# Performance work log

Measured on AMD Instinct MI355X. Metric: run time of the kernel, lower is better.

The kernel has to match this reference:

```python
import jax, jax.numpy as jnp
import numpy as np

LOSS_WEIGHT = 1.0  # init kwarg


def _cdist2(a, b):
    # Euclidean (p=2) pairwise distances via Gram trick: avoids [n,m,d] tensor.
    d2 = (jnp.sum(a * a, axis=1)[:, None]
          + jnp.sum(b * b, axis=1)[None, :]
          - 2.0 * (a @ b.T))
    return jnp.sqrt(jnp.maximum(d2, 0.0))


def _clamp_comb(f, g):
    # Composition of clamp maps x -> clip(x, lo, hi); g is applied after f.
    lf, hf = f
    lg, hg = g
    return jnp.clip(lf, lg, hg), jnp.clip(hf, lg, hg)


def _frechet(pred, target):
    c = _cdist2(pred, target)                      # [n, m]
    # First DP row: running max of c[0, :].
    row0 = jax.lax.associative_scan(jnp.maximum, c[0])

    def row_update(prev, c_row):
        # ca[i,j] = max(min(ca[i-1,j], ca[i,j-1], ca[i-1,j-1]), c[i,j])
        # For fixed i this is d[j] = clip(d[j-1], lo=c[i,j], hi=max(b[j], c[i,j]))
        # with b[j] = min(prev[j], prev[j-1]); clamp composition is associative,
        # so the whole row is a parallel associative scan (wavefront-free form).
        d0 = jnp.maximum(prev[0], c_row[0])        # ca[i,0]
        lo = c_row[1:]
        hi = jnp.maximum(jnp.minimum(prev[1:], prev[:-1]), lo)
        lo_all = jnp.concatenate([d0[None], lo])   # element 0 is the constant map d0
        hi_all = jnp.concatenate([d0[None], hi])
        lo_s, _ = jax.lax.associative_scan(_clamp_comb, (lo_all, hi_all))
        return lo_s, None

    last_row, _ = jax.lax.scan(row_update, row0, c[1:])
    return last_row[-1]


def setup_inputs() -> dict:
    key = jax.random.key(0)
    k1, k2 = jax.random.split(key)
    pred = jax.random.uniform(k1, (4096, 128), dtype=jnp.float32)
    target = jax.random.uniform(k2, (4096, 128), dtype=jnp.float32)
    return {"pred": pred, "target": target}


def reference(pred, target):
    return LOSS_WEIGHT * _frechet(pred, target)
```

## Files before the change

### kernel.cpp

```cpp
#include <hip/hip_runtime.h>

typedef unsigned short u16;
typedef unsigned int u32;
typedef __bf16 bf16x8 __attribute__((ext_vector_type(8)));
typedef float f32x4 __attribute__((ext_vector_type(4)));

#define N 4096
#define KD 128
#define NSTRIP 16
#define G 4
#define W 256
#define ROWB 512
#define CH 64
#define NCHUNK 64
#define NBLK 65
#define WINROWS 192
#define LDSROWS 200
#define TOTSTEP 4159
#define HUGEV 3.0e38f
#define TS 128
#define PADK 136
#define PSTRIDE 32

__device__ __forceinline__ u16 f2bf(float v) {
  u32 u = __float_as_uint(v);
  u += 0x7fffu + ((u >> 16) & 1u);
  return (u16)(u >> 16);
}
__device__ __forceinline__ float bf2f(u16 b) { return __uint_as_float(((u32)b) << 16); }
__device__ __forceinline__ float bfround(float v) { return bf2f(f2bf(v)); }

__device__ __forceinline__ float dpp_shr1(float oldv, float src) {
  return __int_as_float(__builtin_amdgcn_update_dpp(
      __float_as_int(oldv), __float_as_int(src), 0x138, 0xF, 0xF, false));
}

__device__ __forceinline__ void gload_lds16(const void* g, void* l) {
  __builtin_amdgcn_global_load_lds((const __attribute__((address_space(1))) u32*)g,
                                   (__attribute__((address_space(3))) u32*)l, 16, 0, 0);
}

__global__ __launch_bounds__(256) void norms_kernel(const float* __restrict__ pred,
                                                    const float* __restrict__ tgt,
                                                    float* __restrict__ na, float* __restrict__ nb,
                                                    int* __restrict__ prog) {
  if (blockIdx.x == 0 && threadIdx.x < NSTRIP) prog[threadIdx.x * PSTRIDE] = 0;
  int gw = blockIdx.x * 4 + (threadIdx.x >> 6);
  int lane = threadIdx.x & 63;
  const float* base = (gw < N) ? (pred + (size_t)gw * KD) : (tgt + (size_t)(gw - N) * KD);
  float2 v = ((const float2*)base)[lane];
  float x = bfround(v.x), y = bfround(v.y);
  float s = x * x + y * y;
  #pragma unroll
  for (int off = 32; off > 0; off >>= 1) s += __shfl_xor(s, off);
  if (lane == 0) { if (gw < N) na[gw] = s; else nb[gw - N] = s; }
}

__global__ __launch_bounds__(256) void gemm_kernel(const float* __restrict__ A, const float* __restrict__ B,
                                                   const float* __restrict__ na, const float* __restrict__ nb,
                                                   u16* __restrict__ C2) {
  __shared__ u16 As[TS * PADK];
  __shared__ u16 Bs[TS * PADK];
  const int bi = blockIdx.y, bj = blockIdx.x;
  const int tid = threadIdx.x;
  {
    int row = tid >> 1, half = (tid & 1) * 64;
    const float* ga = A + (size_t)(bi * TS + row) * KD + half;
    const float* gb = B + (size_t)(bj * TS + row) * KD + half;
    u16* la = As + row * PADK + half;
    u16* lb = Bs + row * PADK + half;
    #pragma unroll
    for (int v = 0; v < 16; ++v) {
      float4 fa = ((const float4*)ga)[v];
      float4 fb = ((const float4*)gb)[v];
      *(ushort4*)(la + v * 4) = make_ushort4(f2bf(fa.x), f2bf(fa.y), f2bf(fa.z), f2bf(fa.w));
      *(ushort4*)(lb + v * 4) = make_ushort4(f2bf(fb.x), f2bf(fb.y), f2bf(fb.z), f2bf(fb.w));
    }
  }
  __syncthreads();
  const int wid = tid >> 6, lane = tid & 63;
  const int wr = (wid >> 1) * 64, wc = (wid & 1) * 64;
  const int l15 = lane & 15, l4 = lane >> 4;
  f32x4 acc[4][4] = {};
  #pragma unroll
  for (int ks = 0; ks < 4; ++ks) {
    bf16x8 af[4], bq[4];
    const int ko = ks * 32 + l4 * 8;
    #pragma unroll
    for (int m = 0; m < 4; ++m) af[m] = *(const bf16x8*)(As + (wr + m * 16 + l15) * PADK + ko);
    #pragma unroll
    for (int n = 0; n < 4; ++n) bq[n] = *(const bf16x8*)(Bs + (wc + n * 16 + l15) * PADK + ko);
    #pragma unroll
    for (int m = 0; m < 4; ++m)
      #pragma unroll
      for (int n = 0; n < 4; ++n)
        acc[m][n] = __builtin_amdgcn_mfma_f32_16x16x32_bf16(af[m], bq[n], acc[m][n], 0, 0, 0);
  }
  #pragma unroll
  for (int m = 0; m < 4; ++m) {
    const int r0 = bi * TS + wr + m * 16 + l4 * 4;
    #pragma unroll
    for (int n = 0; n < 4; ++n) {
      const int col = bj * TS + wc + n * 16 + l15;
      const float nbv = nb[col];
      #pragma unroll
      for (int e = 0; e < 4; ++e) {
        const int r = r0 + e;
        float d2v = fmaxf(na[r] + nbv - 2.0f * acc[m][n][e], 0.0f);
        C2[(size_t)r * N + col] = f2bf(d2v);
      }
    }
  }
}

#define STEP_F(CU, EV) { \
  const float c0 = bf2f((CU).x), c1 = bf2f((CU).y), c2 = bf2f((CU).z), c3 = bf2f((CU).w); \
  const float Lc = dpp_shr1((EV), D3); \
  const float h0 = fmaxf(fminf(D0, Lp), c0); \
  const float h1 = fmaxf(fminf(D1, D0), c1); \
  const float h2 = fmaxf(fminf(D2, D1), c2); \
  const float h3 = fmaxf(fminf(D3, D2), c3); \
  float x = __builtin_amdgcn_fmed3f(Lc, c0, h0); D0 = x; \
  x = __builtin_amdgcn_fmed3f(x, c1, h1); D1 = x; \
  x = __builtin_amdgcn_fmed3f(x, c2, h2); D2 = x; \
  x = __builtin_amdgcn_fmed3f(x, c3, h3); D3 = x; \
  Lp = Lc; \
}

__global__ __launch_bounds__(64) void dp_kernel(const u16* __restrict__ C2, float* __restrict__ edge,
                                                int* __restrict__ prog, float* __restrict__ out) {
  __shared__ u16 clds[LDSROWS * W];
  __shared__ __align__(16) float elds[CH];
  __shared__ __align__(16) float eout[CH];
  const int bid = blockIdx.x;
  const int S = ((bid & 7) << 1) | (bid >> 3);
  const int lane = threadIdx.x;
  const u16* cbase = C2 + (size_t)S * W;
  const char* clb = (const char*)clds;
  const bool s0 = (S == 0);
  const bool do_edge = (S != NSTRIP - 1);
  const bool edge63 = do_edge && (lane == 63);

  if (s0) elds[lane] = (lane == 0) ? -HUGEV : HUGEV;

  float D0 = HUGEV, D1 = HUGEV, D2 = HUGEV, D3 = HUGEV, Lp = HUGEV;

  auto STAGE = [&](int q) {
    const int lrow = lane >> 5, lcol = (lane & 31) * 8;
    const u16* g0 = cbase + (size_t)(q * CH + lrow) * N + lcol;
    u16* l0 = clds + (q % 3) * (CH * W);
    #pragma unroll
    for (int n = 0; n < 32; ++n) gload_lds16(g0 + (size_t)(2 * n) * N, l0 + n * 512);
    if ((q % 3) == 0) {
      u16* lm = clds + WINROWS * W;
      #pragma unroll
      for (int n = 0; n < 4; ++n) gload_lds16(g0 + (size_t)(2 * n) * N, lm + n * 512);
    }
  };

  STAGE(0);

  for (int q = 0; q < NBLK; ++q) {
    const int s_lo = q * CH;

    if (S > 0 && s_lo < N) {
      const int needed = (s_lo + CH < N) ? (s_lo + CH) : N;
      const int* pp = prog + (S - 1) * PSTRIDE;
      int it = 0;
      while (__hip_atomic_load(pp, __ATOMIC_RELAXED, __HIP_MEMORY_SCOPE_AGENT) < needed) {
        __builtin_amdgcn_s_sleep(1);
        if (++it > (1 << 22)) break;
      }
      __builtin_amdgcn_fence(__ATOMIC_ACQUIRE, "agent");
      const int er = s_lo + lane;
      float ev = (er < N)
          ? __hip_atomic_load(edge + (size_t)(S - 1) * N + er, __ATOMIC_RELAXED, __HIP_MEMORY_SCOPE_AGENT)
          : HUGEV;
      elds[lane] = ev;
    }
    if (s0 && q == 1 && lane == 0) elds[0] = HUGEV;

    asm volatile("s_waitcnt vmcnt(0)" ::: "memory");
    asm volatile("s_waitcnt lgkmcnt(0)" ::: "memory");
    __builtin_amdgcn_sched_barrier(0);

    if (q + 1 < NCHUNK) STAGE(q + 1);

    int base = ((64 * (q % 3) + WINROWS - lane) % WINROWS) * ROWB + lane * (G * 2);

    if (q != 0 && q != NBLK - 1) {
      #pragma unroll 1
      for (int g = 0; g < 8; ++g) {
        const float4 ea = *(const float4*)(elds + g * 8);
        const float4 eb = *(const float4*)(elds + g * 8 + 4);
        const ushort4 cv0 = *(const ushort4*)(clb + base);
        const ushort4 cv1 = *(const ushort4*)(clb + base + 512);
        const ushort4 cv2 = *(const ushort4*)(clb + base + 1024);
        const ushort4 cv3 = *(const ushort4*)(clb + base + 1536);
        const ushort4 cv4 = *(const ushort4*)(clb + base + 2048);
        const ushort4 cv5 = *(const ushort4*)(clb + base + 2560);
        const ushort4 cv6 = *(const ushort4*)(clb + base + 3072);
        const ushort4 cv7 = *(const ushort4*)(clb + base + 3584);
        base += 8 * ROWB;
        if (base >= WINROWS * ROWB) base -= WINROWS * ROWB;
        float t0, t1, t2, t3, t4, t5, t6, t7;
        STEP_F(cv0, ea.x); t0 = D3;
        STEP_F(cv1, ea.y); t1 = D3;
        STEP_F(cv2, ea.z); t2 = D3;
        STEP_F(cv3, ea.w); t3 = D3;
        STEP_F(cv4, eb.x); t4 = D3;
        STEP_F(cv5, eb.y); t5 = D3;
        STEP_F(cv6, eb.z); t6 = D3;
        STEP_F(cv7, eb.w); t7 = D3;
        if (edge63) {
          eout[g * 8 + 0] = t0; eout[g * 8 + 1] = t1; eout[g * 8 + 2] = t2; eout[g * 8 + 3] = t3;
          eout[g * 8 + 4] = t4; eout[g * 8 + 5] = t5; eout[g * 8 + 6] = t6; eout[g * 8 + 7] = t7;
        }
      }
    } else {
      int a2 = base;
      for (int s = s_lo; s < s_lo + CH; ++s) {
        const ushort4 cuv = *(const ushort4*)(clb + a2);
        a2 += ROWB;
        if (a2 >= WINROWS * ROWB) a2 -= WINROWS * ROWB;
        const float ev = elds[s & (CH - 1)];
        const float c0 = bf2f(cuv.x), c1 = bf2f(cuv.y), c2 = bf2f(cuv.z), c3 = bf2f(cuv.w);
        const float Lc = dpp_shr1(ev, D3);
        const float h0 = fmaxf(fminf(D0, Lp), c0);
        const float h1 = fmaxf(fminf(D1, D0), c1);
        const float h2 = fmaxf(fminf(D2, D1), c2);
        const float h3 = fmaxf(fminf(D3, D2), c3);
        float x = __builtin_amdgcn_fmed3f(Lc, c0, h0);
        const float n0 = x;
        x = __builtin_amdgcn_fmed3f(x, c1, h1);
        const float n1 = x;
        x = __builtin_amdgcn_fmed3f(x, c2, h2);
        const float n2 = x;
        x = __builtin_amdgcn_fmed3f(x, c3, h3);
        const float n3 = x;
        const int ii = s - lane;
        const bool act = (u32)ii < (u32)N;
        Lp = (s0 && lane == 0) ? HUGEV : Lc;
        if (act) { D0 = n0; D1 = n1; D2 = n2; D3 = n3; }
        if (do_edge && act && lane == 63) eout[s - s_lo] = n3;
      }
    }

    if (do_edge) {
      asm volatile("s_waitcnt lgkmcnt(0)" ::: "memory");
      __builtin_amdgcn_sched_barrier(0);
      const int r = s_lo - 63 + lane;
      if (r >= 0 && r < N) {
        const float v = eout[lane];
        __hip_atomic_store(edge + (size_t)S * N + r, v, __ATOMIC_RELAXED, __HIP_MEMORY_SCOPE_AGENT);
      }
      asm volatile("s_waitcnt vmcnt(0)" ::: "memory");
      const int done = ((s_lo + CH < TOTSTEP) ? (s_lo + CH) : TOTSTEP) - 63;
      if (lane == 0)
        __hip_atomic_store(prog + S * PSTRIDE, done, __ATOMIC_RELEASE, __HIP_MEMORY_SCOPE_AGENT);
    }
  }

  if (S == NSTRIP - 1 && lane == 63) out[0] = sqrtf(fmaxf(D3, 0.0f));
}

extern "C" void kernel_launch(void* const* d_in, const int* in_sizes, int n_in,
                              void* d_out, int out_size, void* d_ws, size_t ws_size,
                              hipStream_t stream) {
  const float* pred = (const float*)d_in[0];
  const float* tgt  = (const float*)d_in[1];
  char* ws = (char*)d_ws;
  u16* C2   = (u16*)ws;
  float* na = (float*)(ws + (size_t)N * N * 2);
  float* nb = na + N;
  float* edge = nb + N;
  int* prog = (int*)(edge + (size_t)NSTRIP * N);
  float* out = (float*)d_out;

  hipLaunchKernelGGL(norms_kernel, dim3(2048), dim3(256), 0, stream, pred, tgt, na, nb, prog);
  hipLaunchKernelGGL(gemm_kernel, dim3(32, 32), dim3(256), 0, stream, pred, tgt, na, nb, C2);
  hipLaunchKernelGGL(dp_kernel, dim3(NSTRIP), dim3(64), 0, stream, C2, edge, prog, out);
}
```

Before: 608.3 us.

## Pair DP strips per workgroup with LDS edge handoff and smaller chunks

The wavefront DP is restructured so each workgroup runs two adjacent 256-column strips as two waves. The boundary column passes between them through an LDS ring with workgroup-scope counters, and only every other strip boundary goes through global memory with agent-scope atomics. Chunk size drops from 64 to 32 rows to shorten pipeline fill latency, and the inner loop is software-pipelined with double-buffered LDS loads. This is meant to cut global synchronisation latency on the DP critical path, at the cost of more chunk iterations, intra-block spin-waits, and added handshake complexity.

```diff
diff --git a/kernel.cpp b/kernel.cpp
--- a/kernel.cpp
+++ b/kernel.cpp
@@ -7,16 +7,14 @@
 
 #define N 4096
 #define KD 128
-#define NSTRIP 16
 #define G 4
 #define W 256
-#define ROWB 512
-#define CH 64
-#define NCHUNK 64
-#define NBLK 65
-#define WINROWS 192
-#define LDSROWS 200
+#define CH 32
+#define NCHUNK 128
+#define NBLK 130
 #define TOTSTEP 4159
+#define WINROWS 128
+#define WINB 65536
 #define HUGEV 3.0e38f
 #define TS 128
 #define PADK 136
@@ -44,7 +42,7 @@
                                                     const float* __restrict__ tgt,
                                                     float* __restrict__ na, float* __restrict__ nb,
                                                     int* __restrict__ prog) {
-  if (blockIdx.x == 0 && threadIdx.x < NSTRIP) prog[threadIdx.x * PSTRIDE] = 0;
+  if (blockIdx.x == 0 && threadIdx.x < 16) prog[threadIdx.x * PSTRIDE] = 0;
   int gw = blockIdx.x * 4 + (threadIdx.x >> 6);
   int lane = threadIdx.x & 63;
   const float* base = (gw < N) ? (pred + (size_t)gw * KD) : (tgt + (size_t)(gw - N) * KD);
@@ -127,32 +125,79 @@
   Lp = Lc; \
 }
 
-__global__ __launch_bounds__(64) void dp_kernel(const u16* __restrict__ C2, float* __restrict__ edge,
-                                                int* __restrict__ prog, float* __restrict__ out) {
-  __shared__ u16 clds[LDSROWS * W];
-  __shared__ __align__(16) float elds[CH];
-  __shared__ __align__(16) float eout[CH];
-  const int bid = blockIdx.x;
-  const int S = ((bid & 7) << 1) | (bid >> 3);
-  const int lane = threadIdx.x;
+#define LDGRP(IX, GG) { \
+  const int eo = (s_lo + 8 * (GG)) & emask; \
+  ea2[IX] = *(const float4*)(esrc + eo); \
+  eb2[IX] = *(const float4*)(esrc + eo + 4); \
+  cv[IX][0] = *(const ushort4*)(clb + cbs); \
+  cv[IX][1] = *(const ushort4*)(clb + cbs + 512); \
+  cv[IX][2] = *(const ushort4*)(clb + cbs + 1024); \
+  cv[IX][3] = *(const ushort4*)(clb + cbs + 1536); \
+  cv[IX][4] = *(const ushort4*)(clb + cbs + 2048); \
+  cv[IX][5] = *(const ushort4*)(clb + cbs + 2560); \
+  cv[IX][6] = *(const ushort4*)(clb + cbs + 3072); \
+  cv[IX][7] = *(const ushort4*)(clb + cbs + 3584); \
+  cbs += 4096; if (cbs >= WINB) cbs -= WINB; \
+}
+
+#define CGRP(IX) { \
+  float t0, t1, t2, t3, t4, t5, t6, t7; \
+  STEP_F(cv[IX][0], ea2[IX].x); t0 = D3; \
+  STEP_F(cv[IX][1], ea2[IX].y); t1 = D3; \
+  STEP_F(cv[IX][2], ea2[IX].z); t2 = D3; \
+  STEP_F(cv[IX][3], ea2[IX].w); t3 = D3; \
+  STEP_F(cv[IX][4], eb2[IX].x); t4 = D3; \
+  STEP_F(cv[IX][5], eb2[IX].y); t5 = D3; \
+  STEP_F(cv[IX][6], eb2[IX].z); t6 = D3; \
+  STEP_F(cv[IX][7], eb2[IX].w); t7 = D3; \
+  if (wr63) { \
+    *(float*)((char*)ringw + ( ewb       & 511)) = t0; \
+    *(float*)((char*)ringw + ((ewb +  4) & 511)) = t1; \
+    *(float*)((char*)ringw + ((ewb +  8) & 511)) = t2; \
+    *(float*)((char*)ringw + ((ewb + 12) & 511)) = t3; \
+    *(float*)((char*)ringw + ((ewb + 16) & 511)) = t4; \
+    *(float*)((char*)ringw + ((ewb + 20) & 511)) = t5; \
+    *(float*)((char*)ringw + ((ewb + 24) & 511)) = t6; \
+    *(float*)((char*)ringw + ((ewb + 28) & 511)) = t7; \
+  } \
+  ewb += 32; \
+}
+
+__global__ __launch_bounds__(128) void dp_kernel(const u16* __restrict__ C2, float* __restrict__ edgeG,
+                                                 int* __restrict__ progG, float* __restrict__ out) {
+  __shared__ u16 winbuf[2][136 * 256];
+  __shared__ __align__(16) float ering0[128];
+  __shared__ __align__(16) float ering1[128];
+  __shared__ __align__(16) float einG[32];
+  __shared__ int prodcnt0, conscnt0;
+
+  const int w = blockIdx.x;
+  const int tid = threadIdx.x, wv = tid >> 6, lane = tid & 63;
+  const int S = 2 * w + wv;
   const u16* cbase = C2 + (size_t)S * W;
-  const char* clb = (const char*)clds;
+  u16* win = winbuf[wv];
+  const char* clb = (const char*)win;
+  float* ringw = wv ? ering1 : ering0;
+  const bool prodrole = (wv == 0) || (w < 7);
+  const bool wr63 = prodrole && (lane == 63);
+  float* esrc = wv ? ering0 : einG;
+  const int emask = wv ? 127 : 31;
   const bool s0 = (S == 0);
-  const bool do_edge = (S != NSTRIP - 1);
-  const bool edge63 = do_edge && (lane == 63);
-
-  if (s0) elds[lane] = (lane == 0) ? -HUGEV : HUGEV;
+
+  if (tid == 0) { prodcnt0 = 0; conscnt0 = 0; }
+  if (w == 0 && wv == 0 && lane < 32) einG[lane] = (lane == 0) ? -HUGEV : HUGEV;
+  __syncthreads();
 
   float D0 = HUGEV, D1 = HUGEV, D2 = HUGEV, D3 = HUGEV, Lp = HUGEV;
 
-  auto STAGE = [&](int q) {
+  auto STAGE = [&](int c) {
     const int lrow = lane >> 5, lcol = (lane & 31) * 8;
-    const u16* g0 = cbase + (size_t)(q * CH + lrow) * N + lcol;
-    u16* l0 = clds + (q % 3) * (CH * W);
-    #pragma unroll
-    for (int n = 0; n < 32; ++n) gload_lds16(g0 + (size_t)(2 * n) * N, l0 + n * 512);
-    if ((q % 3) == 0) {
-      u16* lm = clds + WINROWS * W;
+    const u16* g0 = cbase + (size_t)(c * CH + lrow) * N + lcol;
+    u16* l0 = win + ((c * CH) & 127) * 256;
+    #pragma unroll
+    for (int n = 0; n < 16; ++n) gload_lds16(g0 + (size_t)(2 * n) * N, l0 + n * 512);
+    if (((c * CH) & 127) == 0) {
+      u16* lm = win + 128 * 256;
       #pragma unroll
       for (int n = 0; n < 4; ++n) gload_lds16(g0 + (size_t)(2 * n) * N, lm + n * 512);
     }
@@ -162,69 +207,77 @@
 
   for (int q = 0; q < NBLK; ++q) {
     const int s_lo = q * CH;
-
-    if (S > 0 && s_lo < N) {
-      const int needed = (s_lo + CH < N) ? (s_lo + CH) : N;
-      const int* pp = prog + (S - 1) * PSTRIDE;
+    const int s_hi = (s_lo + CH < TOTSTEP) ? (s_lo + CH) : TOTSTEP;
+
+    if (q <= 127) {
+      if (wv == 1) {
+        int it = 0;
+        while (__hip_atomic_load(&prodcnt0, __ATOMIC_ACQUIRE, __HIP_MEMORY_SCOPE_WORKGROUP) < q + 3) {
+          __builtin_amdgcn_s_sleep(1);
+          if (++it > (1 << 22)) break;
+        }
+      } else if (w > 0) {
+        if (lane == 0) {
+          int it = 0;
+          int* pg = progG + (w - 1) * PSTRIDE;
+          while (__hip_atomic_fetch_add(pg, 0, __ATOMIC_RELAXED, __HIP_MEMORY_SCOPE_AGENT) < q + 1) {
+            __builtin_amdgcn_s_sleep(2);
+            if (++it > (1 << 22)) break;
+          }
+        }
+      }
+    }
+    if (wv == 0 && q >= 5) {
       int it = 0;
-      while (__hip_atomic_load(pp, __ATOMIC_RELAXED, __HIP_MEMORY_SCOPE_AGENT) < needed) {
+      while (__hip_atomic_load(&conscnt0, __ATOMIC_RELAXED, __HIP_MEMORY_SCOPE_WORKGROUP) < q - 4) {
         __builtin_amdgcn_s_sleep(1);
         if (++it > (1 << 22)) break;
       }
-      __builtin_amdgcn_fence(__ATOMIC_ACQUIRE, "agent");
-      const int er = s_lo + lane;
-      float ev = (er < N)
-          ? __hip_atomic_load(edge + (size_t)(S - 1) * N + er, __ATOMIC_RELAXED, __HIP_MEMORY_SCOPE_AGENT)
-          : HUGEV;
-      elds[lane] = ev;
-    }
-    if (s0 && q == 1 && lane == 0) elds[0] = HUGEV;
+    }
 
     asm volatile("s_waitcnt vmcnt(0)" ::: "memory");
+    __builtin_amdgcn_sched_barrier(0);
+
+    const int nst = (q + 1 < NCHUNK) ? ((((q + 1) * CH) & 127) == 0 ? 20 : 16) : 0;
+    if (wv == 0 && w > 0 && q <= 127) {
+      float ev = HUGEV;
+      if (lane < 32)
+        ev = __hip_atomic_load(edgeG + (size_t)(w - 1) * N + s_lo + lane,
+                               __ATOMIC_RELAXED, __HIP_MEMORY_SCOPE_AGENT);
+      __builtin_amdgcn_sched_barrier(0);
+      if (q + 1 < NCHUNK) STAGE(q + 1);
+      __builtin_amdgcn_sched_barrier(0);
+      if (nst == 16)      asm volatile("s_waitcnt vmcnt(16)" ::: "memory");
+      else if (nst == 20) asm volatile("s_waitcnt vmcnt(20)" ::: "memory");
+      else                asm volatile("s_waitcnt vmcnt(0)" ::: "memory");
+      if (lane < 32) einG[lane] = ev;
+    } else {
+      if (q + 1 < NCHUNK) STAGE(q + 1);
+    }
+    if (s0 && wv == 0 && q == 1 && lane == 0) einG[0] = HUGEV;
     asm volatile("s_waitcnt lgkmcnt(0)" ::: "memory");
     __builtin_amdgcn_sched_barrier(0);
 
-    if (q + 1 < NCHUNK) STAGE(q + 1);
-
-    int base = ((64 * (q % 3) + WINROWS - lane) % WINROWS) * ROWB + lane * (G * 2);
-
-    if (q != 0 && q != NBLK - 1) {
-      #pragma unroll 1
-      for (int g = 0; g < 8; ++g) {
-        const float4 ea = *(const float4*)(elds + g * 8);
-        const float4 eb = *(const float4*)(elds + g * 8 + 4);
-        const ushort4 cv0 = *(const ushort4*)(clb + base);
-        const ushort4 cv1 = *(const ushort4*)(clb + base + 512);
-        const ushort4 cv2 = *(const ushort4*)(clb + base + 1024);
-        const ushort4 cv3 = *(const ushort4*)(clb + base + 1536);
-        const ushort4 cv4 = *(const ushort4*)(clb + base + 2048);
-        const ushort4 cv5 = *(const ushort4*)(clb + base + 2560);
-        const ushort4 cv6 = *(const ushort4*)(clb + base + 3072);
-        const ushort4 cv7 = *(const ushort4*)(clb + base + 3584);
-        base += 8 * ROWB;
-        if (base >= WINROWS * ROWB) base -= WINROWS * ROWB;
-        float t0, t1, t2, t3, t4, t5, t6, t7;
-        STEP_F(cv0, ea.x); t0 = D3;
-        STEP_F(cv1, ea.y); t1 = D3;
-        STEP_F(cv2, ea.z); t2 = D3;
-        STEP_F(cv3, ea.w); t3 = D3;
-        STEP_F(cv4, eb.x); t4 = D3;
-        STEP_F(cv5, eb.y); t5 = D3;
-        STEP_F(cv6, eb.z); t6 = D3;
-        STEP_F(cv7, eb.w); t7 = D3;
-        if (edge63) {
-          eout[g * 8 + 0] = t0; eout[g * 8 + 1] = t1; eout[g * 8 + 2] = t2; eout[g * 8 + 3] = t3;
-          eout[g * 8 + 4] = t4; eout[g * 8 + 5] = t5; eout[g * 8 + 6] = t6; eout[g * 8 + 7] = t7;
-        }
-      }
+    u32 cbs = (((u32)(s_lo - lane)) & 127) * 512 + lane * 8;
+    int ewb = (((s_lo - 63) & 127)) * 4;
+
+    if (q >= 2 && q <= 127) {
+      ushort4 cv[2][8];
+      float4 ea2[2], eb2[2];
+      LDGRP(0, 0)
+      LDGRP(1, 1)
+      CGRP(0)
+      LDGRP(0, 2)
+      CGRP(1)
+      LDGRP(1, 3)
+      CGRP(0)
+      CGRP(1)
     } else {
-      int a2 = base;
-      for (int s = s_lo; s < s_lo + CH; ++s) {
-        const ushort4 cuv = *(const ushort4*)(clb + a2);
-        a2 += ROWB;
-        if (a2 >= WINROWS * ROWB) a2 -= WINROWS * ROWB;
-        const float ev = elds[s & (CH - 1)];
-        const float c0 = bf2f(cuv.x), c1 = bf2f(cuv.y), c2 = bf2f(cuv.z), c3 = bf2f(cuv.w);
+      for (int s = s_lo; s < s_hi; ++s) {
+        const ushort4 cu = *(const ushort4*)(clb + cbs);
+        cbs += 512; if (cbs >= WINB) cbs -= WINB;
+        const float ev = esrc[s & emask];
+        const float c0 = bf2f(cu.x), c1 = bf2f(cu.y), c2 = bf2f(cu.z), c3 = bf2f(cu.w);
         const float Lc = dpp_shr1(ev, D3);
         const float h0 = fmaxf(fminf(D0, Lp), c0);
         const float h1 = fmaxf(fminf(D1, D0), c1);
@@ -242,26 +295,34 @@
         const bool act = (u32)ii < (u32)N;
         Lp = (s0 && lane == 0) ? HUGEV : Lc;
         if (act) { D0 = n0; D1 = n1; D2 = n2; D3 = n3; }
-        if (do_edge && act && lane == 63) eout[s - s_lo] = n3;
-      }
-    }
-
-    if (do_edge) {
-      asm volatile("s_waitcnt lgkmcnt(0)" ::: "memory");
-      __builtin_amdgcn_sched_barrier(0);
-      const int r = s_lo - 63 + lane;
-      if (r >= 0 && r < N) {
-        const float v = eout[lane];
-        __hip_atomic_store(edge + (size_t)S * N + r, v, __ATOMIC_RELAXED, __HIP_MEMORY_SCOPE_AGENT);
-      }
-      asm volatile("s_waitcnt vmcnt(0)" ::: "memory");
-      const int done = ((s_lo + CH < TOTSTEP) ? (s_lo + CH) : TOTSTEP) - 63;
+        const int ie = s - 63;
+        if (wr63 && ie >= 0) *(float*)((char*)ringw + ((ie & 127) * 4)) = n3;
+      }
+    }
+
+    if (wv == 0) {
       if (lane == 0)
-        __hip_atomic_store(prog + S * PSTRIDE, done, __ATOMIC_RELEASE, __HIP_MEMORY_SCOPE_AGENT);
+        __hip_atomic_store(&prodcnt0, q + 1, __ATOMIC_RELEASE, __HIP_MEMORY_SCOPE_WORKGROUP);
+    } else {
+      if (lane == 0)
+        __hip_atomic_store(&conscnt0, q + 1, __ATOMIC_RELAXED, __HIP_MEMORY_SCOPE_WORKGROUP);
+      if (w < 7 && q >= 2) {
+        const int rb = q - 2;
+        asm volatile("s_waitcnt lgkmcnt(0)" ::: "memory");
+        if (lane < 32) {
+          const float v = ering1[(rb & 3) * 32 + lane];
+          __hip_atomic_store(edgeG + (size_t)w * N + rb * 32 + lane, v,
+                             __ATOMIC_RELAXED, __HIP_MEMORY_SCOPE_AGENT);
+        }
+        asm volatile("s_waitcnt vmcnt(0)" ::: "memory");
+        if (lane == 0)
+          (void)__hip_atomic_exchange(progG + w * PSTRIDE, rb + 1,
+                                      __ATOMIC_RELAXED, __HIP_MEMORY_SCOPE_AGENT);
+      }
     }
   }
 
-  if (S == NSTRIP - 1 && lane == 63) out[0] = sqrtf(fmaxf(D3, 0.0f));
+  if (wv == 1 && w == 7 && lane == 63) out[0] = sqrtf(fmaxf(D3, 0.0f));
 }
 
 extern "C" void kernel_launch(void* const* d_in, const int* in_sizes, int n_in,
@@ -273,11 +334,11 @@
   u16* C2   = (u16*)ws;
   float* na = (float*)(ws + (size_t)N * N * 2);
   float* nb = na + N;
-  float* edge = nb + N;
-  int* prog = (int*)(edge + (size_t)NSTRIP * N);
+  float* edgeG = nb + N;
+  int* progG = (int*)(edgeG + (size_t)16 * N);
   float* out = (float*)d_out;
 
-  hipLaunchKernelGGL(norms_kernel, dim3(2048), dim3(256), 0, stream, pred, tgt, na, nb, prog);
+  hipLaunchKernelGGL(norms_kernel, dim3(2048), dim3(256), 0, stream, pred, tgt, na, nb, progG);
   hipLaunchKernelGGL(gemm_kernel, dim3(32, 32), dim3(256), 0, stream, pred, tgt, na, nb, C2);
-  hipLaunchKernelGGL(dp_kernel, dim3(NSTRIP), dim3(64), 0, stream, C2, edge, prog, out);
-}
+  hipLaunchKernelGGL(dp_kernel, dim3(8), dim3(128), 0, stream, C2, edgeG, progG, out);
+}
```

Result: slower. 680.5 us (+11.9%).

## Double chunk size to 128 with two-buffer LDS window and software-pipelined LDS loads

Applied to the files above, without the earlier changes.

Doubles the DP chunk from 64 to 128 anti-diagonal steps, replacing the triple-buffered 192-row LDS window with a double-buffered 256-row window. This halves the number of inter-strip handshakes. The inner loop now software-pipelines LDS reads by loading the next group of eight rows while the current group is computed. Progress is tracked as a chunk count polled by a single lane, and the edge-value global loads are issued before the wait on the staging loads. The larger chunk means each strip waits longer before its neighbour can start, which lengthens pipeline fill across the 16 strips. It also raises LDS use to about 135 KB.

```diff
diff --git a/kernel.cpp b/kernel.cpp
--- a/kernel.cpp
+++ b/kernel.cpp
@@ -10,13 +10,11 @@
 #define NSTRIP 16
 #define G 4
 #define W 256
-#define ROWB 512
-#define CH 64
-#define NCHUNK 64
-#define NBLK 65
-#define WINROWS 192
-#define LDSROWS 200
+#define CH 128
+#define NBLK 33
 #define TOTSTEP 4159
+#define WROWS 256
+#define WINB 131072
 #define HUGEV 3.0e38f
 #define TS 128
 #define PADK 136
@@ -127,32 +125,63 @@
   Lp = Lc; \
 }
 
-__global__ __launch_bounds__(64) void dp_kernel(const u16* __restrict__ C2, float* __restrict__ edge,
-                                                int* __restrict__ prog, float* __restrict__ out) {
-  __shared__ u16 clds[LDSROWS * W];
+#define LDGRP_(EA, EB, CV, GG) { \
+  EA = *(const float4*)(elds + 8 * (GG)); \
+  EB = *(const float4*)(elds + 8 * (GG) + 4); \
+  CV##0 = *(const ushort4*)(clb + cbs); \
+  CV##1 = *(const ushort4*)(clb + cbs + 512); \
+  CV##2 = *(const ushort4*)(clb + cbs + 1024); \
+  CV##3 = *(const ushort4*)(clb + cbs + 1536); \
+  CV##4 = *(const ushort4*)(clb + cbs + 2048); \
+  CV##5 = *(const ushort4*)(clb + cbs + 2560); \
+  CV##6 = *(const ushort4*)(clb + cbs + 3072); \
+  CV##7 = *(const ushort4*)(clb + cbs + 3584); \
+  cbs += 4096; if (cbs >= WINB) cbs -= WINB; \
+}
+
+#define CGRP_(EA, EB, CV) { \
+  float t0, t1, t2, t3, t4, t5, t6, t7; \
+  STEP_F(CV##0, EA.x); t0 = D3; \
+  STEP_F(CV##1, EA.y); t1 = D3; \
+  STEP_F(CV##2, EA.z); t2 = D3; \
+  STEP_F(CV##3, EA.w); t3 = D3; \
+  STEP_F(CV##4, EB.x); t4 = D3; \
+  STEP_F(CV##5, EB.y); t5 = D3; \
+  STEP_F(CV##6, EB.z); t6 = D3; \
+  STEP_F(CV##7, EB.w); t7 = D3; \
+  if (e63) { \
+    eout[eg + 0] = t0; eout[eg + 1] = t1; eout[eg + 2] = t2; eout[eg + 3] = t3; \
+    eout[eg + 4] = t4; eout[eg + 5] = t5; eout[eg + 6] = t6; eout[eg + 7] = t7; \
+  } \
+  eg += 8; \
+}
+
+__global__ __launch_bounds__(64) void dp_kernel(const u16* __restrict__ C2, float* __restrict__ edgeG,
+                                                int* __restrict__ progG, float* __restrict__ out) {
+  __shared__ u16 win[(WROWS + 8) * W];
   __shared__ __align__(16) float elds[CH];
   __shared__ __align__(16) float eout[CH];
   const int bid = blockIdx.x;
   const int S = ((bid & 7) << 1) | (bid >> 3);
   const int lane = threadIdx.x;
   const u16* cbase = C2 + (size_t)S * W;
-  const char* clb = (const char*)clds;
+  const char* clb = (const char*)win;
   const bool s0 = (S == 0);
   const bool do_edge = (S != NSTRIP - 1);
-  const bool edge63 = do_edge && (lane == 63);
-
-  if (s0) elds[lane] = (lane == 0) ? -HUGEV : HUGEV;
+  const bool e63 = do_edge && (lane == 63);
+
+  if (s0) { elds[lane] = (lane == 0) ? -HUGEV : HUGEV; elds[64 + lane] = HUGEV; }
 
   float D0 = HUGEV, D1 = HUGEV, D2 = HUGEV, D3 = HUGEV, Lp = HUGEV;
 
-  auto STAGE = [&](int q) {
+  auto STAGE = [&](int c) {
     const int lrow = lane >> 5, lcol = (lane & 31) * 8;
-    const u16* g0 = cbase + (size_t)(q * CH + lrow) * N + lcol;
-    u16* l0 = clds + (q % 3) * (CH * W);
-    #pragma unroll
-    for (int n = 0; n < 32; ++n) gload_lds16(g0 + (size_t)(2 * n) * N, l0 + n * 512);
-    if ((q % 3) == 0) {
-      u16* lm = clds + WINROWS * W;
+    const u16* g0 = cbase + (size_t)(c * CH + lrow) * N + lcol;
+    u16* l0 = win + ((c & 1) * CH) * W;
+    #pragma unroll
+    for (int n = 0; n < 64; ++n) gload_lds16(g0 + (size_t)(2 * n) * N, l0 + n * 512);
+    if ((c & 1) == 0) {
+      u16* lm = win + WROWS * W;
       #pragma unroll
       for (int n = 0; n < 4; ++n) gload_lds16(g0 + (size_t)(2 * n) * N, lm + n * 512);
     }
@@ -162,69 +191,66 @@
 
   for (int q = 0; q < NBLK; ++q) {
     const int s_lo = q * CH;
-
-    if (S > 0 && s_lo < N) {
-      const int needed = (s_lo + CH < N) ? (s_lo + CH) : N;
-      const int* pp = prog + (S - 1) * PSTRIDE;
-      int it = 0;
-      while (__hip_atomic_load(pp, __ATOMIC_RELAXED, __HIP_MEMORY_SCOPE_AGENT) < needed) {
-        __builtin_amdgcn_s_sleep(1);
-        if (++it > (1 << 22)) break;
+    const int s_hi = (s_lo + CH < TOTSTEP) ? (s_lo + CH) : TOTSTEP;
+
+    if (S > 0 && q <= 31) {
+      if (lane == 0) {
+        int tgt = q + 2; if (tgt > NBLK) tgt = NBLK;
+        int it = 0; int* pg = progG + (S - 1) * PSTRIDE;
+        while (__hip_atomic_fetch_add(pg, 0, __ATOMIC_RELAXED, __HIP_MEMORY_SCOPE_AGENT) < tgt) {
+          __builtin_amdgcn_s_sleep(1);
+          if (++it > (1 << 22)) break;
+        }
       }
       __builtin_amdgcn_fence(__ATOMIC_ACQUIRE, "agent");
-      const int er = s_lo + lane;
-      float ev = (er < N)
-          ? __hip_atomic_load(edge + (size_t)(S - 1) * N + er, __ATOMIC_RELAXED, __HIP_MEMORY_SCOPE_AGENT)
-          : HUGEV;
-      elds[lane] = ev;
-    }
+    }
+
+    float ev0 = HUGEV, ev1 = HUGEV;
+    const bool eload = (S > 0 && q <= 31);
+    if (eload) {
+      ev0 = __hip_atomic_load(edgeG + (size_t)(S - 1) * N + s_lo + lane,
+                              __ATOMIC_RELAXED, __HIP_MEMORY_SCOPE_AGENT);
+      ev1 = __hip_atomic_load(edgeG + (size_t)(S - 1) * N + s_lo + 64 + lane,
+                              __ATOMIC_RELAXED, __HIP_MEMORY_SCOPE_AGENT);
+    }
+
+    if (eload) { asm volatile("s_waitcnt vmcnt(2)" ::: "memory"); }
+    else       { asm volatile("s_waitcnt vmcnt(0)" ::: "memory"); }
+    __builtin_amdgcn_sched_barrier(0);
+
+    if (eload) { elds[lane] = ev0; elds[64 + lane] = ev1; }
     if (s0 && q == 1 && lane == 0) elds[0] = HUGEV;
-
-    asm volatile("s_waitcnt vmcnt(0)" ::: "memory");
+    __builtin_amdgcn_sched_barrier(0);
+
+    if (q < 31) STAGE(q + 1);
+
     asm volatile("s_waitcnt lgkmcnt(0)" ::: "memory");
     __builtin_amdgcn_sched_barrier(0);
 
-    if (q + 1 < NCHUNK) STAGE(q + 1);
-
-    int base = ((64 * (q % 3) + WINROWS - lane) % WINROWS) * ROWB + lane * (G * 2);
-
-    if (q != 0 && q != NBLK - 1) {
+    u32 cbs = (((u32)(s_lo - lane)) & 255) * 512 + lane * (G * 2);
+    int eg = 0;
+
+    if (q >= 1 && q <= 31) {
+      float4 eaA, ebA, eaB, ebB;
+      ushort4 cA0, cA1, cA2, cA3, cA4, cA5, cA6, cA7;
+      ushort4 cB0, cB1, cB2, cB3, cB4, cB5, cB6, cB7;
+      LDGRP_(eaA, ebA, cA, 0)
+      LDGRP_(eaB, ebB, cB, 1)
       #pragma unroll 1
-      for (int g = 0; g < 8; ++g) {
-        const float4 ea = *(const float4*)(elds + g * 8);
-        const float4 eb = *(const float4*)(elds + g * 8 + 4);
-        const ushort4 cv0 = *(const ushort4*)(clb + base);
-        const ushort4 cv1 = *(const ushort4*)(clb + base + 512);
-        const ushort4 cv2 = *(const ushort4*)(clb + base + 1024);
-        const ushort4 cv3 = *(const ushort4*)(clb + base + 1536);
-        const ushort4 cv4 = *(const ushort4*)(clb + base + 2048);
-        const ushort4 cv5 = *(const ushort4*)(clb + base + 2560);
-        const ushort4 cv6 = *(const ushort4*)(clb + base + 3072);
-        const ushort4 cv7 = *(const ushort4*)(clb + base + 3584);
-        base += 8 * ROWB;
-        if (base >= WINROWS * ROWB) base -= WINROWS * ROWB;
-        float t0, t1, t2, t3, t4, t5, t6, t7;
-        STEP_F(cv0, ea.x); t0 = D3;
-        STEP_F(cv1, ea.y); t1 = D3;
-        STEP_F(cv2, ea.z); t2 = D3;
-        STEP_F(cv3, ea.w); t3 = D3;
-        STEP_F(cv4, eb.x); t4 = D3;
-        STEP_F(cv5, eb.y); t5 = D3;
-        STEP_F(cv6, eb.z); t6 = D3;
-        STEP_F(cv7, eb.w); t7 = D3;
-        if (edge63) {
-          eout[g * 8 + 0] = t0; eout[g * 8 + 1] = t1; eout[g * 8 + 2] = t2; eout[g * 8 + 3] = t3;
-          eout[g * 8 + 4] = t4; eout[g * 8 + 5] = t5; eout[g * 8 + 6] = t6; eout[g * 8 + 7] = t7;
-        }
+      for (int k = 0; k < 7; ++k) {
+        CGRP_(eaA, ebA, cA)
+        LDGRP_(eaA, ebA, cA, 2 * k + 2)
+        CGRP_(eaB, ebB, cB)
+        LDGRP_(eaB, ebB, cB, 2 * k + 3)
       }
+      CGRP_(eaA, ebA, cA)
+      CGRP_(eaB, ebB, cB)
     } else {
-      int a2 = base;
-      for (int s = s_lo; s < s_lo + CH; ++s) {
-        const ushort4 cuv = *(const ushort4*)(clb + a2);
-        a2 += ROWB;
-        if (a2 >= WINROWS * ROWB) a2 -= WINROWS * ROWB;
+      for (int s = s_lo; s < s_hi; ++s) {
+        const ushort4 cu = *(const ushort4*)(clb + cbs);
+        cbs += 512; if (cbs >= WINB) cbs -= WINB;
         const float ev = elds[s & (CH - 1)];
-        const float c0 = bf2f(cuv.x), c1 = bf2f(cuv.y), c2 = bf2f(cuv.z), c3 = bf2f(cuv.w);
+        const float c0 = bf2f(cu.x), c1 = bf2f(cu.y), c2 = bf2f(cu.z), c3 = bf2f(cu.w);
         const float Lc = dpp_shr1(ev, D3);
         const float h0 = fmaxf(fminf(D0, Lp), c0);
         const float h1 = fmaxf(fminf(D1, D0), c1);
@@ -242,22 +268,22 @@
         const bool act = (u32)ii < (u32)N;
         Lp = (s0 && lane == 0) ? HUGEV : Lc;
         if (act) { D0 = n0; D1 = n1; D2 = n2; D3 = n3; }
-        if (do_edge && act && lane == 63) eout[s - s_lo] = n3;
+        if (e63 && act) eout[s - s_lo] = n3;
       }
     }
 
     if (do_edge) {
       asm volatile("s_waitcnt lgkmcnt(0)" ::: "memory");
       __builtin_amdgcn_sched_barrier(0);
-      const int r = s_lo - 63 + lane;
-      if (r >= 0 && r < N) {
-        const float v = eout[lane];
-        __hip_atomic_store(edge + (size_t)S * N + r, v, __ATOMIC_RELAXED, __HIP_MEMORY_SCOPE_AGENT);
-      }
+      const float v0 = eout[lane], v1 = eout[64 + lane];
+      const int r0 = s_lo - 63 + lane, r1 = r0 + 64;
+      if (r0 >= 0 && r0 < N)
+        __hip_atomic_store(edgeG + (size_t)S * N + r0, v0, __ATOMIC_RELAXED, __HIP_MEMORY_SCOPE_AGENT);
+      if (r1 >= 0 && r1 < N)
+        __hip_atomic_store(edgeG + (size_t)S * N + r1, v1, __ATOMIC_RELAXED, __HIP_MEMORY_SCOPE_AGENT);
       asm volatile("s_waitcnt vmcnt(0)" ::: "memory");
-      const int done = ((s_lo + CH < TOTSTEP) ? (s_lo + CH) : TOTSTEP) - 63;
       if (lane == 0)
-        __hip_atomic_store(prog + S * PSTRIDE, done, __ATOMIC_RELEASE, __HIP_MEMORY_SCOPE_AGENT);
+        __hip_atomic_store(progG + S * PSTRIDE, q + 1, __ATOMIC_RELAXED, __HIP_MEMORY_SCOPE_AGENT);
     }
   }
 
@@ -273,11 +299,11 @@
   u16* C2   = (u16*)ws;
   float* na = (float*)(ws + (size_t)N * N * 2);
   float* nb = na + N;
-  float* edge = nb + N;
-  int* prog = (int*)(edge + (size_t)NSTRIP * N);
+  float* edgeG = nb + N;
+  int* progG = (int*)(edgeG + (size_t)NSTRIP * N);
   float* out = (float*)d_out;
 
-  hipLaunchKernelGGL(norms_kernel, dim3(2048), dim3(256), 0, stream, pred, tgt, na, nb, prog);
+  hipLaunchKernelGGL(norms_kernel, dim3(2048), dim3(256), 0, stream, pred, tgt, na, nb, progG);
   hipLaunchKernelGGL(gemm_kernel, dim3(32, 32), dim3(256), 0, stream, pred, tgt, na, nb, C2);
-  hipLaunchKernelGGL(dp_kernel, dim3(NSTRIP), dim3(64), 0, stream, C2, edge, prog, out);
-}
+  hipLaunchKernelGGL(dp_kernel, dim3(NSTRIP), dim3(64), 0, stream, C2, edgeG, progG, out);
+}
```

After: 774.9 us. 1.27x slower.
